# Kernel tuning notes

Measured on AMD Instinct MI355X. Metric: run time of the kernel, lower is better.

## Reference

```python
import jax, jax.numpy as jnp
import numpy as np

N = 16384      # total nodes (hits)
K = 8          # n_neighbors
NB = 8         # number of graphs in batch
IN_C = 6       # in_channels
HID = 128      # hidden_channels
NCLS = 3       # num_classes
SLOPE = 0.2    # GATv2 leaky_relu negative_slope
BIG = 1e30     # mask value for cross-graph pairs


def setup_inputs() -> dict:
    key = jax.random.key(0)
    ks = jax.random.split(key, 32)
    coord = jax.random.normal(ks[0], (N, 3), dtype=jnp.float32)
    feat = jax.random.normal(ks[1], (N, IN_C), dtype=jnp.float32)
    batch = jnp.sort(jax.random.randint(ks[2], (N,), 0, NB)).astype(jnp.int32)

    def lin_w(k, fan_in, fan_out):
        return (jax.random.normal(k, (fan_in, fan_out), dtype=jnp.float32)
                * np.float32(1.0 / np.sqrt(fan_in)))

    inp = {"coord": coord, "feat": feat, "batch": batch}
    dims = [IN_C, HID, HID]  # input dim of each of the 3 GATv2 layers
    kidx = 3
    for l, din in enumerate(dims):
        inp[f"Wl{l}"] = lin_w(ks[kidx], din, HID); kidx += 1
        inp[f"bl{l}"] = jnp.zeros((HID,), jnp.float32)
        inp[f"Wr{l}"] = lin_w(ks[kidx], din, HID); kidx += 1
        inp[f"br{l}"] = jnp.zeros((HID,), jnp.float32)
        inp[f"att{l}"] = (jax.random.normal(ks[kidx], (HID,), dtype=jnp.float32)
                          * np.float32(1.0 / np.sqrt(HID))); kidx += 1
        inp[f"bias{l}"] = jnp.zeros((HID,), jnp.float32)
    inp["Wf"] = lin_w(ks[kidx], HID, NCLS)
    inp["bf"] = jnp.zeros((NCLS,), jnp.float32)
    return inp


def knn_idx(coord, batch):
    # pairwise squared distances, masked so neighbors stay within the same graph
    d2 = jnp.sum((coord[:, None, :] - coord[None, :, :]) ** 2, axis=-1)  # [N,N]
    d2 = jnp.where(batch[:, None] == batch[None, :], d2, BIG)
    _, idx = jax.lax.top_k(-d2, K)  # [N,K] nearest (includes self at dist 0)
    return idx


def gatv2_layer(x, idx, Wl, bl, Wr, br, att, bias):
    xl = x @ Wl + bl                         # [N,H] source transform
    xr = x @ Wr + br                         # [N,H] target transform
    g = xl[idx]                              # [N,K,H] gather neighbor features
    e = jax.nn.leaky_relu(g + xr[:, None, :], SLOPE)
    logits = e @ att                         # [N,K] attention scores
    alpha = jax.nn.softmax(logits, axis=1)   # softmax over each node's K nbrs
    return jnp.einsum('nk,nkh->nh', alpha, g) + bias


def reference(coord, feat, batch,
              Wl0, bl0, Wr0, br0, att0, bias0,
              Wl1, bl1, Wr1, br1, att1, bias1,
              Wl2, bl2, Wr2, br2, att2, bias2,
              Wf, bf):
    idx = knn_idx(coord, batch)
    x = jax.nn.relu(gatv2_layer(feat, idx, Wl0, bl0, Wr0, br0, att0, bias0))
    x = jax.nn.relu(gatv2_layer(x, idx, Wl1, bl1, Wr1, br1, att1, bias1))
    x = jax.nn.relu(gatv2_layer(x, idx, Wl2, bl2, Wr2, br2, att2, bias2))
    return x @ Wf + bf
```

## Files before the change

kernel.cpp:

```cpp
#include <hip/hip_runtime.h>
#include <hip/hip_bf16.h>
#include <float.h>
#include <limits.h>

#define NNODES 16384
#define KNB 8
#define HIDC 128
#define KNN_CAP 2528

__device__ __forceinline__ float wave_sum(float x) {
  x += __int_as_float(__builtin_amdgcn_update_dpp(0, __float_as_int(x), 0xB1, 0xF, 0xF, true));
  x += __int_as_float(__builtin_amdgcn_update_dpp(0, __float_as_int(x), 0x4E, 0xF, 0xF, true));
  x += __int_as_float(__builtin_amdgcn_update_dpp(0, __float_as_int(x), 0x124, 0xF, 0xF, true));
  x += __int_as_float(__builtin_amdgcn_update_dpp(0, __float_as_int(x), 0x128, 0xF, 0xF, true));
  float r0 = __int_as_float(__builtin_amdgcn_readlane(__float_as_int(x), 0));
  float r1 = __int_as_float(__builtin_amdgcn_readlane(__float_as_int(x), 16));
  float r2 = __int_as_float(__builtin_amdgcn_readlane(__float_as_int(x), 32));
  float r3 = __int_as_float(__builtin_amdgcn_readlane(__float_as_int(x), 48));
  return (r0 + r1) + (r2 + r3);
}

__device__ __forceinline__ float wave_min_f32(float x) {
  x = fminf(x, __int_as_float(__builtin_amdgcn_update_dpp(0, __float_as_int(x), 0xB1, 0xF, 0xF, true)));
  x = fminf(x, __int_as_float(__builtin_amdgcn_update_dpp(0, __float_as_int(x), 0x4E, 0xF, 0xF, true)));
  x = fminf(x, __int_as_float(__builtin_amdgcn_update_dpp(0, __float_as_int(x), 0x124, 0xF, 0xF, true)));
  x = fminf(x, __int_as_float(__builtin_amdgcn_update_dpp(0, __float_as_int(x), 0x128, 0xF, 0xF, true)));
  float r0 = __int_as_float(__builtin_amdgcn_readlane(__float_as_int(x), 0));
  float r1 = __int_as_float(__builtin_amdgcn_readlane(__float_as_int(x), 16));
  float r2 = __int_as_float(__builtin_amdgcn_readlane(__float_as_int(x), 32));
  float r3 = __int_as_float(__builtin_amdgcn_readlane(__float_as_int(x), 48));
  return fminf(fminf(r0, r1), fminf(r2, r3));
}

__device__ __forceinline__ float dist2(float ax, float ay, float az,
                                       float bx, float by, float bz) {
  float dx = ax - bx, dy = ay - by, dz = az - bz;
  return fmaf(dz, dz, fmaf(dy, dy, dx * dx));
}

#define INS8V(_d, a0, a1, a2, a3, a4, a5, a6, a7)  \
  do {                                             \
    a7 = __builtin_amdgcn_fmed3f(_d, a6, a7);      \
    a6 = __builtin_amdgcn_fmed3f(_d, a5, a6);      \
    a5 = __builtin_amdgcn_fmed3f(_d, a4, a5);      \
    a4 = __builtin_amdgcn_fmed3f(_d, a3, a4);      \
    a3 = __builtin_amdgcn_fmed3f(_d, a2, a3);      \
    a2 = __builtin_amdgcn_fmed3f(_d, a1, a2);      \
    a1 = __builtin_amdgcn_fmed3f(_d, a0, a1);      \
    a0 = fminf(a0, _d);                            \
  } while (0)

__device__ __forceinline__ float merge_T(float l0, float l1, float l2, float l3,
                                         float l4, float l5, float l6, float l7,
                                         int lane) {
  float T = 0.f;
  #pragma unroll
  for (int r = 0; r < KNB; ++r) {
    float m = wave_min_f32(l0);
    T = m;
    unsigned long long msk = __ballot(l0 == m);
    int p = (int)__builtin_ctzll(msk);
    if (lane == p) { l0 = l1; l1 = l2; l2 = l3; l3 = l4; l4 = l5; l5 = l6; l6 = l7; l7 = FLT_MAX; }
  }
  return T;
}

__device__ void knn_global_single(const float* __restrict__ coord,
                                  float qx, float qy, float qz,
                                  int s, int e, int lane,
                                  int* __restrict__ knn_row) {
  float l0 = FLT_MAX, l1 = FLT_MAX, l2 = FLT_MAX, l3 = FLT_MAX,
        l4 = FLT_MAX, l5 = FLT_MAX, l6 = FLT_MAX, l7 = FLT_MAX;
  for (int base = s; base < e; base += 64) {
    int j = base + lane;
    bool ok = j < e;
    int jc = ok ? j : s;
    float d = dist2(coord[jc*3+0], coord[jc*3+1], coord[jc*3+2], qx, qy, qz);
    d = ok ? d : FLT_MAX;
    INS8V(d, l0, l1, l2, l3, l4, l5, l6, l7);
  }
  float T = merge_T(l0, l1, l2, l3, l4, l5, l6, l7, lane);
  unsigned long long lt = (1ull << lane) - 1ull;
  int cnt = 0;
  for (int base = s; base < e; base += 64) {
    int j = base + lane;
    bool ok = j < e;
    int jc = ok ? j : s;
    float d = dist2(coord[jc*3+0], coord[jc*3+1], coord[jc*3+2], qx, qy, qz);
    bool win = ok && (d <= T);
    unsigned long long msk = __ballot(win);
    if (msk) {
      int slot = cnt + __popcll(msk & lt);
      if (win && slot < KNB) knn_row[slot] = j;
      cnt += __popcll(msk);
    }
  }
}

__global__ void seg_kernel(const int* __restrict__ batch, int* __restrict__ seg) {
  int b = threadIdx.x;
  if (b > 8) return;
  int lo = 0, hi = NNODES;
  while (lo < hi) { int m = (lo + hi) >> 1; if (batch[m] < b) lo = m + 1; else hi = m; }
  seg[b] = lo;
}

__global__ __launch_bounds__(512, 8) void knnlin_kernel(
    const float* __restrict__ coord, const int* __restrict__ batch,
    const float* __restrict__ feat,
    const float* __restrict__ Wl0, const float* __restrict__ bl0,
    const float* __restrict__ Wr0, const float* __restrict__ br0,
    const int* __restrict__ seg,
    int* __restrict__ knn, float* __restrict__ xl, float* __restrict__ xr) {
  __shared__ float xs[KNN_CAP];
  __shared__ float ys[KNN_CAP];
  __shared__ float zs[KNN_CAP];
  int t = threadIdx.x;
  int lane = t & 63;
  int wid = t >> 6;
  int n0 = blockIdx.x * 16;

  int b0 = batch[n0];
  int blast = batch[n0 + 15];
  int smin = seg[b0];
  int emax = seg[blast + 1];
  int win_end = min(emax, smin + KNN_CAP);
  int cnt_fill = win_end - smin;

  for (int i = t; i < cnt_fill; i += 512) {
    const float* cp = coord + (size_t)(smin + i) * 3;
    xs[i] = cp[0]; ys[i] = cp[1]; zs[i] = cp[2];
  }
  __syncthreads();

  int nA = n0 + wid * 2, nB = nA + 1;
  int bA = batch[nA], bB = batch[nB];
  int sA = seg[bA], eA = seg[bA + 1];
  bool fast = (bA == bB) && (eA - smin <= KNN_CAP);

  float ax = coord[nA*3+0], ay = coord[nA*3+1], az = coord[nA*3+2];
  float bx = coord[nB*3+0], by = coord[nB*3+1], bz = coord[nB*3+2];

  if (fast) {
    int lo_i = sA - smin;
    int M = eA - sA;
    int F4 = M >> 8;

    float a0 = FLT_MAX, a1 = FLT_MAX, a2 = FLT_MAX, a3 = FLT_MAX,
          a4 = FLT_MAX, a5 = FLT_MAX, a6 = FLT_MAX, a7 = FLT_MAX;
    float b0r = FLT_MAX, b1 = FLT_MAX, b2 = FLT_MAX, b3 = FLT_MAX,
          b4 = FLT_MAX, b5 = FLT_MAX, b6 = FLT_MAX, b7 = FLT_MAX;
    {
      for (int it = 0; it < F4; ++it) {
        int base = lo_i + (it << 8) + lane;
        #pragma unroll
        for (int q = 0; q < 4; ++q) {
          int i = base + (q << 6);
          float cxv = xs[i], cyv = ys[i], czv = zs[i];
          float dA = dist2(cxv, cyv, czv, ax, ay, az);
          float dB = dist2(cxv, cyv, czv, bx, by, bz);
          INS8V(dA, a0, a1, a2, a3, a4, a5, a6, a7);
          INS8V(dB, b0r, b1, b2, b3, b4, b5, b6, b7);
        }
      }
      for (int base = F4 << 8; base < M; base += 64) {
        int lix = base + lane;
        bool ok = lix < M;
        int i = ok ? (lo_i + lix) : lo_i;
        float cxv = xs[i], cyv = ys[i], czv = zs[i];
        float dA = dist2(cxv, cyv, czv, ax, ay, az);
        float dB = dist2(cxv, cyv, czv, bx, by, bz);
        dA = ok ? dA : FLT_MAX;
        dB = ok ? dB : FLT_MAX;
        INS8V(dA, a0, a1, a2, a3, a4, a5, a6, a7);
        INS8V(dB, b0r, b1, b2, b3, b4, b5, b6, b7);
      }
    }

    float TA = merge_T(a0, a1, a2, a3, a4, a5, a6, a7, lane);
    float TB = merge_T(b0r, b1, b2, b3, b4, b5, b6, b7, lane);

    unsigned long long lt = (1ull << lane) - 1ull;
    int cntA = 0, cntB = 0;
    {
      for (int it = 0; it < F4 && (cntA < KNB || cntB < KNB); ++it) {
        int base = lo_i + (it << 8) + lane;
        int g0 = sA + (it << 8) + lane;
        #pragma unroll
        for (int q = 0; q < 4; ++q) {
          int i = base + (q << 6);
          int gidx = g0 + (q << 6);
          float cxv = xs[i], cyv = ys[i], czv = zs[i];
          float dA = dist2(cxv, cyv, czv, ax, ay, az);
          float dB = dist2(cxv, cyv, czv, bx, by, bz);
          unsigned long long mA = __ballot(dA <= TA);
          if (mA) {
            int slot = cntA + __popcll(mA & lt);
            if ((dA <= TA) && slot < KNB) knn[nA*KNB + slot] = gidx;
            cntA += __popcll(mA);
          }
          unsigned long long mB = __ballot(dB <= TB);
          if (mB) {
            int slot = cntB + __popcll(mB & lt);
            if ((dB <= TB) && slot < KNB) knn[nB*KNB + slot] = gidx;
            cntB += __popcll(mB);
          }
        }
      }
      for (int base = F4 << 8; base < M && (cntA < KNB || cntB < KNB); base += 64) {
        int lix = base + lane;
        bool ok = lix < M;
        int i = ok ? (lo_i + lix) : lo_i;
        float cxv = xs[i], cyv = ys[i], czv = zs[i];
        float dA = dist2(cxv, cyv, czv, ax, ay, az);
        float dB = dist2(cxv, cyv, czv, bx, by, bz);
        int gidx = sA + lix;
        bool wA = ok && (dA <= TA);
        bool wB = ok && (dB <= TB);
        unsigned long long mA = __ballot(wA);
        if (mA) {
          int slot = cntA + __popcll(mA & lt);
          if (wA && slot < KNB) knn[nA*KNB + slot] = gidx;
          cntA += __popcll(mA);
        }
        unsigned long long mB = __ballot(wB);
        if (mB) {
          int slot = cntB + __popcll(mB & lt);
          if (wB && slot < KNB) knn[nB*KNB + slot] = gidx;
          cntB += __popcll(mB);
        }
      }
    }
  } else {
    int sB2 = seg[bB], eB2 = seg[bB + 1];
    knn_global_single(coord, ax, ay, az, sA, eA, lane, knn + (size_t)nA * KNB);
    knn_global_single(coord, bx, by, bz, sB2, eB2, lane, knn + (size_t)nB * KNB);
  }

  {
    int cg = t & 63;
    bool isR = cg >= 32;
    const float* W  = isR ? Wr0 : Wl0;
    const float* bi = isR ? br0 : bl0;
    float* dst      = isR ? xr : xl;
    int wc = (cg & 31) * 4;
    float4 w0 = *(const float4*)(W + 0 * HIDC + wc);
    float4 w1 = *(const float4*)(W + 1 * HIDC + wc);
    float4 w2 = *(const float4*)(W + 2 * HIDC + wc);
    float4 w3 = *(const float4*)(W + 3 * HIDC + wc);
    float4 w4 = *(const float4*)(W + 4 * HIDC + wc);
    float4 w5 = *(const float4*)(W + 5 * HIDC + wc);
    float4 bb = *(const float4*)(bi + wc);
    #pragma unroll
    for (int s2 = 0; s2 < 2; ++s2) {
      int node = n0 + wid * 2 + s2;
      const float* fr = feat + (size_t)node * 6;
      float f0 = fr[0], f1 = fr[1], f2 = fr[2], f3 = fr[3], f4 = fr[4], f5 = fr[5];
      float4 acc = make_float4(0.f, 0.f, 0.f, 0.f);
      acc.x = fmaf(f0, w0.x, acc.x); acc.y = fmaf(f0, w0.y, acc.y);
      acc.z = fmaf(f0, w0.z, acc.z); acc.w = fmaf(f0, w0.w, acc.w);
      acc.x = fmaf(f1, w1.x, acc.x); acc.y = fmaf(f1, w1.y, acc.y);
      acc.z = fmaf(f1, w1.z, acc.z); acc.w = fmaf(f1, w1.w, acc.w);
      acc.x = fmaf(f2, w2.x, acc.x); acc.y = fmaf(f2, w2.y, acc.y);
      acc.z = fmaf(f2, w2.z, acc.z); acc.w = fmaf(f2, w2.w, acc.w);
      acc.x = fmaf(f3, w3.x, acc.x); acc.y = fmaf(f3, w3.y, acc.y);
      acc.z = fmaf(f3, w3.z, acc.z); acc.w = fmaf(f3, w3.w, acc.w);
      acc.x = fmaf(f4, w4.x, acc.x); acc.y = fmaf(f4, w4.y, acc.y);
      acc.z = fmaf(f4, w4.z, acc.z); acc.w = fmaf(f4, w4.w, acc.w);
      acc.x = fmaf(f5, w5.x, acc.x); acc.y = fmaf(f5, w5.y, acc.y);
      acc.z = fmaf(f5, w5.z, acc.z); acc.w = fmaf(f5, w5.w, acc.w);
      float4 o;
      o.x = acc.x + bb.x; o.y = acc.y + bb.y;
      o.z = acc.z + bb.z; o.w = acc.w + bb.w;
      *(float4*)(dst + (size_t)node * HIDC + wc) = o;
    }
  }
}

__global__ __launch_bounds__(256) void lin2_kernel(
    const float* __restrict__ x,
    const float* __restrict__ Wl, const float* __restrict__ bl,
    const float* __restrict__ Wr, const float* __restrict__ br,
    float* __restrict__ xl, float* __restrict__ xr) {
  __shared__ float xshm[16 * HIDC];
  int t = threadIdx.x;
  int node0 = blockIdx.x * 16;
  for (int i = t; i < 16 * HIDC; i += 256) xshm[i] = x[node0 * HIDC + i];
  __syncthreads();
  int cg = t & 63;
  int ng = t >> 6;
  int c0 = cg * 4;
  bool isR = (c0 >= HIDC);
  const float* W    = isR ? Wr : Wl;
  const float* bias = isR ? br : bl;
  float* dst        = isR ? xr : xl;
  int wc = isR ? (c0 - HIDC) : c0;

  float4 acc[4];
  #pragma unroll
  for (int nn = 0; nn < 4; ++nn) acc[nn] = make_float4(0.f, 0.f, 0.f, 0.f);

  for (int k0 = 0; k0 < HIDC; k0 += 4) {
    float4 xv[4];
    #pragma unroll
    for (int nn = 0; nn < 4; ++nn)
      xv[nn] = *(const float4*)&xshm[(ng * 4 + nn) * HIDC + k0];
    #pragma unroll
    for (int q = 0; q < 4; ++q) {
      float4 w = *(const float4*)(W + (size_t)(k0 + q) * HIDC + wc);
      #pragma unroll
      for (int nn = 0; nn < 4; ++nn) {
        float xq = (q == 0) ? xv[nn].x : (q == 1) ? xv[nn].y : (q == 2) ? xv[nn].z : xv[nn].w;
        acc[nn].x = fmaf(xq, w.x, acc[nn].x);
        acc[nn].y = fmaf(xq, w.y, acc[nn].y);
        acc[nn].z = fmaf(xq, w.z, acc[nn].z);
        acc[nn].w = fmaf(xq, w.w, acc[nn].w);
      }
    }
  }
  float4 b4 = *(const float4*)(bias + wc);
  #pragma unroll
  for (int nn = 0; nn < 4; ++nn) {
    int node = node0 + ng * 4 + nn;
    float4 o;
    o.x = acc[nn].x + b4.x; o.y = acc[nn].y + b4.y;
    o.z = acc[nn].z + b4.z; o.w = acc[nn].w + b4.w;
    *(float4*)(dst + (size_t)node * HIDC + wc) = o;
  }
}

template<bool FINAL>
__global__ __launch_bounds__(256) void gat_attn_kernel(
    const float* __restrict__ xl, const float* __restrict__ xr,
    const int* __restrict__ knn, const float* __restrict__ att,
    const float* __restrict__ bias, float* __restrict__ xout,
    const float* __restrict__ Wf, const float* __restrict__ bf,
    float* __restrict__ out) {
  int wid = threadIdx.x >> 6;
  int lane = threadIdx.x & 63;
  int n = blockIdx.x * 4 + wid;
  int c0 = 2 * lane, c1 = 2 * lane + 1;
  float2 xr2 = *(const float2*)(xr + (size_t)n * HIDC + c0);
  float2 a2  = *(const float2*)(att + c0);
  int myj = (lane < KNB) ? knn[n * KNB + lane] : 0;
  float g0[8], g1[8], lg[8];
  #pragma unroll
  for (int k = 0; k < 8; ++k) {
    int j = __builtin_amdgcn_readlane(myj, k);
    float2 g = *(const float2*)(xl + (size_t)j * HIDC + c0);
    g0[k] = g.x; g1[k] = g.y;
    float e0 = g.x + xr2.x; e0 = (e0 > 0.f) ? e0 : 0.2f * e0;
    float e1 = g.y + xr2.y; e1 = (e1 > 0.f) ? e1 : 0.2f * e1;
    lg[k] = wave_sum(e0 * a2.x + e1 * a2.y);
  }
  float mx = lg[0];
  #pragma unroll
  for (int k = 1; k < 8; ++k) mx = fmaxf(mx, lg[k]);
  float ssum = 0.f, w[8];
  #pragma unroll
  for (int k = 0; k < 8; ++k) { w[k] = __expf(lg[k] - mx); ssum += w[k]; }
  float inv = 1.f / ssum;
  float o0 = 0.f, o1 = 0.f;
  #pragma unroll
  for (int k = 0; k < 8; ++k) { o0 += w[k] * g0[k]; o1 += w[k] * g1[k]; }
  o0 = fmaxf(fmaf(o0, inv, bias[c0]), 0.f);
  o1 = fmaxf(fmaf(o1, inv, bias[c1]), 0.f);
  if (!FINAL) {
    float2 o; o.x = o0; o.y = o1;
    *(float2*)(xout + (size_t)n * HIDC + c0) = o;
  } else {
    #pragma unroll
    for (int cls = 0; cls < 3; ++cls) {
      float p = wave_sum(o0 * Wf[c0 * 3 + cls] + o1 * Wf[c1 * 3 + cls]);
      if (lane == 0) out[n * 3 + cls] = p + bf[cls];
    }
  }
}

extern "C" void kernel_launch(void* const* d_in, const int* in_sizes, int n_in,
                              void* d_out, int out_size, void* d_ws, size_t ws_size,
                              hipStream_t stream) {
  const float* coord = (const float*)d_in[0];
  const float* feat  = (const float*)d_in[1];
  const int*   batch = (const int*)d_in[2];
  const float* Wl0 = (const float*)d_in[3];
  const float* bl0 = (const float*)d_in[4];
  const float* Wr0 = (const float*)d_in[5];
  const float* br0 = (const float*)d_in[6];
  const float* att0  = (const float*)d_in[7];
  const float* bias0 = (const float*)d_in[8];
  const float* Wl1 = (const float*)d_in[9];
  const float* bl1 = (const float*)d_in[10];
  const float* Wr1 = (const float*)d_in[11];
  const float* br1 = (const float*)d_in[12];
  const float* att1  = (const float*)d_in[13];
  const float* bias1 = (const float*)d_in[14];
  const float* Wl2 = (const float*)d_in[15];
  const float* bl2 = (const float*)d_in[16];
  const float* Wr2 = (const float*)d_in[17];
  const float* br2 = (const float*)d_in[18];
  const float* att2  = (const float*)d_in[19];
  const float* bias2 = (const float*)d_in[20];
  const float* Wf = (const float*)d_in[21];
  const float* bf = (const float*)d_in[22];
  float* out = (float*)d_out;

  char* ws = (char*)d_ws;
  int*   knn = (int*)ws;
  float* xl  = (float*)(ws + (512 << 10));
  float* xr  = xl + (size_t)NNODES * HIDC;
  float* xb0 = xr + (size_t)NNODES * HIDC;
  float* xb1 = xb0 + (size_t)NNODES * HIDC;
  int*   seg = (int*)xb1;

  seg_kernel<<<1, 16, 0, stream>>>(batch, seg);
  knnlin_kernel<<<NNODES / 16, 512, 0, stream>>>(coord, batch, feat,
                                                 Wl0, bl0, Wr0, br0, seg, knn, xl, xr);
  gat_attn_kernel<false><<<NNODES / 4, 256, 0, stream>>>(xl, xr, knn, att0, bias0, xb0,
                                                         nullptr, nullptr, nullptr);

  lin2_kernel<<<NNODES / 16, 256, 0, stream>>>(xb0, Wl1, bl1, Wr1, br1, xl, xr);
  gat_attn_kernel<false><<<NNODES / 4, 256, 0, stream>>>(xl, xr, knn, att1, bias1, xb1,
                                                         nullptr, nullptr, nullptr);

  lin2_kernel<<<NNODES / 16, 256, 0, stream>>>(xb1, Wl2, bl2, Wr2, br2, xl, xr);
  gat_attn_kernel<true><<<NNODES / 4, 256, 0, stream>>>(xl, xr, knn, att2, bias2, nullptr,
                                                        Wf, bf, out);
}
```

Baseline: 138.2 us.

## Process four query nodes per wave in KNN to reuse LDS candidate loads

Each wave now handles four query nodes instead of two, so every candidate coordinate read from LDS is reused across four distance computations. Blocks cover 32 nodes, which halves the grid and the number of per-block LDS fills. The 4x-unrolled first-pass loop is replaced with a simple 64-stride loop, and the second pass exits early once all four queries have their K neighbours. Keeping four sorted top-8 lists per lane raises register pressure, so launch bounds drop to 4 blocks per CU, and the halved grid gives less parallelism.

Result: slower. 157.8 us (+14.1%).

```diff
diff --git a/kernel.cpp b/kernel.cpp
--- a/kernel.cpp
+++ b/kernel.cpp
@@ -105,7 +105,7 @@
   seg[b] = lo;
 }
 
-__global__ __launch_bounds__(512, 8) void knnlin_kernel(
+__global__ __launch_bounds__(512, 4) void knnlin_kernel(
     const float* __restrict__ coord, const int* __restrict__ batch,
     const float* __restrict__ feat,
     const float* __restrict__ Wl0, const float* __restrict__ bl0,
@@ -118,10 +118,10 @@
   int t = threadIdx.x;
   int lane = t & 63;
   int wid = t >> 6;
-  int n0 = blockIdx.x * 16;
+  int n0 = blockIdx.x * 32;
 
   int b0 = batch[n0];
-  int blast = batch[n0 + 15];
+  int blast = batch[n0 + 31];
   int smin = seg[b0];
   int emax = seg[blast + 1];
   int win_end = min(emax, smin + KNN_CAP);
@@ -133,108 +133,95 @@
   }
   __syncthreads();
 
-  int nA = n0 + wid * 2, nB = nA + 1;
-  int bA = batch[nA], bB = batch[nB];
-  int sA = seg[bA], eA = seg[bA + 1];
-  bool fast = (bA == bB) && (eA - smin <= KNN_CAP);
-
-  float ax = coord[nA*3+0], ay = coord[nA*3+1], az = coord[nA*3+2];
-  float bx = coord[nB*3+0], by = coord[nB*3+1], bz = coord[nB*3+2];
+  int nQ0 = n0 + wid * 4, nQ1 = nQ0 + 1, nQ2 = nQ0 + 2, nQ3 = nQ0 + 3;
+  int bQ0 = batch[nQ0], bQ3 = batch[nQ3];
+  int sA = seg[bQ0], eA = seg[bQ0 + 1];
+  bool fast = (bQ0 == bQ3) && (eA - smin <= KNN_CAP);
+
+  float q0x = coord[nQ0*3+0], q0y = coord[nQ0*3+1], q0z = coord[nQ0*3+2];
+  float q1x = coord[nQ1*3+0], q1y = coord[nQ1*3+1], q1z = coord[nQ1*3+2];
+  float q2x = coord[nQ2*3+0], q2y = coord[nQ2*3+1], q2z = coord[nQ2*3+2];
+  float q3x = coord[nQ3*3+0], q3y = coord[nQ3*3+1], q3z = coord[nQ3*3+2];
 
   if (fast) {
     int lo_i = sA - smin;
     int M = eA - sA;
-    int F4 = M >> 8;
+    int Mf = M & ~63;
 
     float a0 = FLT_MAX, a1 = FLT_MAX, a2 = FLT_MAX, a3 = FLT_MAX,
           a4 = FLT_MAX, a5 = FLT_MAX, a6 = FLT_MAX, a7 = FLT_MAX;
     float b0r = FLT_MAX, b1 = FLT_MAX, b2 = FLT_MAX, b3 = FLT_MAX,
           b4 = FLT_MAX, b5 = FLT_MAX, b6 = FLT_MAX, b7 = FLT_MAX;
-    {
-      for (int it = 0; it < F4; ++it) {
-        int base = lo_i + (it << 8) + lane;
-        #pragma unroll
-        for (int q = 0; q < 4; ++q) {
-          int i = base + (q << 6);
-          float cxv = xs[i], cyv = ys[i], czv = zs[i];
-          float dA = dist2(cxv, cyv, czv, ax, ay, az);
-          float dB = dist2(cxv, cyv, czv, bx, by, bz);
-          INS8V(dA, a0, a1, a2, a3, a4, a5, a6, a7);
-          INS8V(dB, b0r, b1, b2, b3, b4, b5, b6, b7);
-        }
-      }
-      for (int base = F4 << 8; base < M; base += 64) {
-        int lix = base + lane;
-        bool ok = lix < M;
-        int i = ok ? (lo_i + lix) : lo_i;
-        float cxv = xs[i], cyv = ys[i], czv = zs[i];
-        float dA = dist2(cxv, cyv, czv, ax, ay, az);
-        float dB = dist2(cxv, cyv, czv, bx, by, bz);
-        dA = ok ? dA : FLT_MAX;
-        dB = ok ? dB : FLT_MAX;
-        INS8V(dA, a0, a1, a2, a3, a4, a5, a6, a7);
-        INS8V(dB, b0r, b1, b2, b3, b4, b5, b6, b7);
-      }
-    }
-
-    float TA = merge_T(a0, a1, a2, a3, a4, a5, a6, a7, lane);
-    float TB = merge_T(b0r, b1, b2, b3, b4, b5, b6, b7, lane);
+    float c0r = FLT_MAX, c1 = FLT_MAX, c2 = FLT_MAX, c3 = FLT_MAX,
+          c4 = FLT_MAX, c5 = FLT_MAX, c6 = FLT_MAX, c7 = FLT_MAX;
+    float e0r = FLT_MAX, e1 = FLT_MAX, e2 = FLT_MAX, e3 = FLT_MAX,
+          e4 = FLT_MAX, e5 = FLT_MAX, e6 = FLT_MAX, e7 = FLT_MAX;
+    for (int base = 0; base < Mf; base += 64) {
+      int i = lo_i + base + lane;
+      float cxv = xs[i], cyv = ys[i], czv = zs[i];
+      float d0 = dist2(cxv, cyv, czv, q0x, q0y, q0z);
+      float d1 = dist2(cxv, cyv, czv, q1x, q1y, q1z);
+      float d2v = dist2(cxv, cyv, czv, q2x, q2y, q2z);
+      float d3 = dist2(cxv, cyv, czv, q3x, q3y, q3z);
+      INS8V(d0, a0, a1, a2, a3, a4, a5, a6, a7);
+      INS8V(d1, b0r, b1, b2, b3, b4, b5, b6, b7);
+      INS8V(d2v, c0r, c1, c2, c3, c4, c5, c6, c7);
+      INS8V(d3, e0r, e1, e2, e3, e4, e5, e6, e7);
+    }
+    if (Mf < M) {
+      int lix = Mf + lane;
+      bool ok = lix < M;
+      int i = ok ? (lo_i + lix) : lo_i;
+      float cxv = xs[i], cyv = ys[i], czv = zs[i];
+      float d0 = ok ? dist2(cxv, cyv, czv, q0x, q0y, q0z) : FLT_MAX;
+      float d1 = ok ? dist2(cxv, cyv, czv, q1x, q1y, q1z) : FLT_MAX;
+      float d2v = ok ? dist2(cxv, cyv, czv, q2x, q2y, q2z) : FLT_MAX;
+      float d3 = ok ? dist2(cxv, cyv, czv, q3x, q3y, q3z) : FLT_MAX;
+      INS8V(d0, a0, a1, a2, a3, a4, a5, a6, a7);
+      INS8V(d1, b0r, b1, b2, b3, b4, b5, b6, b7);
+      INS8V(d2v, c0r, c1, c2, c3, c4, c5, c6, c7);
+      INS8V(d3, e0r, e1, e2, e3, e4, e5, e6, e7);
+    }
+
+    float T0 = merge_T(a0, a1, a2, a3, a4, a5, a6, a7, lane);
+    float T1 = merge_T(b0r, b1, b2, b3, b4, b5, b6, b7, lane);
+    float T2 = merge_T(c0r, c1, c2, c3, c4, c5, c6, c7, lane);
+    float T3 = merge_T(e0r, e1, e2, e3, e4, e5, e6, e7, lane);
 
     unsigned long long lt = (1ull << lane) - 1ull;
-    int cntA = 0, cntB = 0;
-    {
-      for (int it = 0; it < F4 && (cntA < KNB || cntB < KNB); ++it) {
-        int base = lo_i + (it << 8) + lane;
-        int g0 = sA + (it << 8) + lane;
-        #pragma unroll
-        for (int q = 0; q < 4; ++q) {
-          int i = base + (q << 6);
-          int gidx = g0 + (q << 6);
-          float cxv = xs[i], cyv = ys[i], czv = zs[i];
-          float dA = dist2(cxv, cyv, czv, ax, ay, az);
-          float dB = dist2(cxv, cyv, czv, bx, by, bz);
-          unsigned long long mA = __ballot(dA <= TA);
-          if (mA) {
-            int slot = cntA + __popcll(mA & lt);
-            if ((dA <= TA) && slot < KNB) knn[nA*KNB + slot] = gidx;
-            cntA += __popcll(mA);
-          }
-          unsigned long long mB = __ballot(dB <= TB);
-          if (mB) {
-            int slot = cntB + __popcll(mB & lt);
-            if ((dB <= TB) && slot < KNB) knn[nB*KNB + slot] = gidx;
-            cntB += __popcll(mB);
-          }
-        }
-      }
-      for (int base = F4 << 8; base < M && (cntA < KNB || cntB < KNB); base += 64) {
-        int lix = base + lane;
-        bool ok = lix < M;
-        int i = ok ? (lo_i + lix) : lo_i;
-        float cxv = xs[i], cyv = ys[i], czv = zs[i];
-        float dA = dist2(cxv, cyv, czv, ax, ay, az);
-        float dB = dist2(cxv, cyv, czv, bx, by, bz);
-        int gidx = sA + lix;
-        bool wA = ok && (dA <= TA);
-        bool wB = ok && (dB <= TB);
-        unsigned long long mA = __ballot(wA);
-        if (mA) {
-          int slot = cntA + __popcll(mA & lt);
-          if (wA && slot < KNB) knn[nA*KNB + slot] = gidx;
-          cntA += __popcll(mA);
-        }
-        unsigned long long mB = __ballot(wB);
-        if (mB) {
-          int slot = cntB + __popcll(mB & lt);
-          if (wB && slot < KNB) knn[nB*KNB + slot] = gidx;
-          cntB += __popcll(mB);
-        }
-      }
-    }
+    int cnt0 = 0, cnt1 = 0, cnt2 = 0, cnt3 = 0;
+#define PASS2Q(dq, Tq, cntq, nq)                                   \
+    {                                                              \
+      bool w = okc && ((dq) <= (Tq));                              \
+      unsigned long long m = __ballot(w);                          \
+      if (m) {                                                     \
+        int slot = cntq + __popcll(m & lt);                        \
+        if (w && slot < KNB) knn[(size_t)(nq)*KNB + slot] = gidx;  \
+        cntq += __popcll(m);                                       \
+      }                                                            \
+    }
+    for (int base = 0; base < M; base += 64) {
+      int lix = base + lane;
+      bool okc = lix < M;
+      int i = okc ? (lo_i + lix) : lo_i;
+      int gidx = sA + lix;
+      float cxv = xs[i], cyv = ys[i], czv = zs[i];
+      float d0 = dist2(cxv, cyv, czv, q0x, q0y, q0z);
+      float d1 = dist2(cxv, cyv, czv, q1x, q1y, q1z);
+      float d2v = dist2(cxv, cyv, czv, q2x, q2y, q2z);
+      float d3 = dist2(cxv, cyv, czv, q3x, q3y, q3z);
+      PASS2Q(d0, T0, cnt0, nQ0);
+      PASS2Q(d1, T1, cnt1, nQ1);
+      PASS2Q(d2v, T2, cnt2, nQ2);
+      PASS2Q(d3, T3, cnt3, nQ3);
+      if (cnt0 >= KNB && cnt1 >= KNB && cnt2 >= KNB && cnt3 >= KNB) break;
+    }
+#undef PASS2Q
   } else {
-    int sB2 = seg[bB], eB2 = seg[bB + 1];
-    knn_global_single(coord, ax, ay, az, sA, eA, lane, knn + (size_t)nA * KNB);
-    knn_global_single(coord, bx, by, bz, sB2, eB2, lane, knn + (size_t)nB * KNB);
+    knn_global_single(coord, q0x, q0y, q0z, seg[batch[nQ0]], seg[batch[nQ0]+1], lane, knn + (size_t)nQ0 * KNB);
+    knn_global_single(coord, q1x, q1y, q1z, seg[batch[nQ1]], seg[batch[nQ1]+1], lane, knn + (size_t)nQ1 * KNB);
+    knn_global_single(coord, q2x, q2y, q2z, seg[batch[nQ2]], seg[batch[nQ2]+1], lane, knn + (size_t)nQ2 * KNB);
+    knn_global_single(coord, q3x, q3y, q3z, seg[batch[nQ3]], seg[batch[nQ3]+1], lane, knn + (size_t)nQ3 * KNB);
   }
 
   {
@@ -252,8 +239,8 @@
     float4 w5 = *(const float4*)(W + 5 * HIDC + wc);
     float4 bb = *(const float4*)(bi + wc);
     #pragma unroll
-    for (int s2 = 0; s2 < 2; ++s2) {
-      int node = n0 + wid * 2 + s2;
+    for (int s2 = 0; s2 < 4; ++s2) {
+      int node = n0 + wid * 4 + s2;
       const float* fr = feat + (size_t)node * 6;
       float f0 = fr[0], f1 = fr[1], f2 = fr[2], f3 = fr[3], f4 = fr[4], f5 = fr[5];
       float4 acc = make_float4(0.f, 0.f, 0.f, 0.f);
@@ -414,7 +401,7 @@
   int*   seg = (int*)xb1;
 
   seg_kernel<<<1, 16, 0, stream>>>(batch, seg);
-  knnlin_kernel<<<NNODES / 16, 512, 0, stream>>>(coord, batch, feat,
+  knnlin_kernel<<<NNODES / 32, 512, 0, stream>>>(coord, batch, feat,
                                                  Wl0, bl0, Wr0, br0, seg, knn, xl, xr);
   gat_attn_kernel<false><<<NNODES / 4, 256, 0, stream>>>(xl, xr, knn, att0, bias0, xb0,
                                                          nullptr, nullptr, nullptr);
```

## Fuse GAT attention with next layer's linear transforms, ping-pong buffers

Applied to the files above, without the earlier changes.

Merges each intermediate GATv2 attention step with the following layer's Wl/Wr projection into one kernel. The aggregated node features stay in shared memory instead of being written to global memory and read back, which also removes two kernel launches. Each block now handles 8 nodes instead of 16 for the linear part, so every weight row is loaded for fewer nodes. Double-buffered xl/xr arrays avoid read-after-write hazards between layers.

New measurement: 142.0 us. 2.8% more time.

```diff
diff --git a/kernel.cpp b/kernel.cpp
--- a/kernel.cpp
+++ b/kernel.cpp
@@ -277,39 +277,77 @@
   }
 }
 
-__global__ __launch_bounds__(256) void lin2_kernel(
-    const float* __restrict__ x,
+__global__ __launch_bounds__(256) void gatlin_kernel(
+    const float* __restrict__ xl_in, const float* __restrict__ xr_in,
+    const int* __restrict__ knn, const float* __restrict__ att,
+    const float* __restrict__ bias,
     const float* __restrict__ Wl, const float* __restrict__ bl,
     const float* __restrict__ Wr, const float* __restrict__ br,
-    float* __restrict__ xl, float* __restrict__ xr) {
-  __shared__ float xshm[16 * HIDC];
+    float* __restrict__ xl_out, float* __restrict__ xr_out) {
+  __shared__ float xshm[8 * HIDC];
   int t = threadIdx.x;
-  int node0 = blockIdx.x * 16;
-  for (int i = t; i < 16 * HIDC; i += 256) xshm[i] = x[node0 * HIDC + i];
+  int wid = t >> 6;
+  int lane = t & 63;
+  int n0 = blockIdx.x * 8;
+  int c0 = 2 * lane, c1 = c0 + 1;
+  float2 a2 = *(const float2*)(att + c0);
+  float2 b2 = *(const float2*)(bias + c0);
+
+  #pragma unroll
+  for (int s = 0; s < 2; ++s) {
+    int nl = wid * 2 + s;
+    int n = n0 + nl;
+    float2 xr2 = *(const float2*)(xr_in + (size_t)n * HIDC + c0);
+    int myj = (lane < KNB) ? knn[n * KNB + lane] : 0;
+    float g0[8], g1[8], lg[8];
+    #pragma unroll
+    for (int k = 0; k < 8; ++k) {
+      int j = __builtin_amdgcn_readlane(myj, k);
+      float2 g = *(const float2*)(xl_in + (size_t)j * HIDC + c0);
+      g0[k] = g.x; g1[k] = g.y;
+      float e0 = g.x + xr2.x; e0 = (e0 > 0.f) ? e0 : 0.2f * e0;
+      float e1 = g.y + xr2.y; e1 = (e1 > 0.f) ? e1 : 0.2f * e1;
+      lg[k] = wave_sum(e0 * a2.x + e1 * a2.y);
+    }
+    float mx = lg[0];
+    #pragma unroll
+    for (int k = 1; k < 8; ++k) mx = fmaxf(mx, lg[k]);
+    float ssum = 0.f, w[8];
+    #pragma unroll
+    for (int k = 0; k < 8; ++k) { w[k] = __expf(lg[k] - mx); ssum += w[k]; }
+    float inv = 1.f / ssum;
+    float o0 = 0.f, o1 = 0.f;
+    #pragma unroll
+    for (int k = 0; k < 8; ++k) { o0 += w[k] * g0[k]; o1 += w[k] * g1[k]; }
+    o0 = fmaxf(fmaf(o0, inv, b2.x), 0.f);
+    o1 = fmaxf(fmaf(o1, inv, b2.y), 0.f);
+    float2 o; o.x = o0; o.y = o1;
+    *(float2*)(&xshm[nl * HIDC + c0]) = o;
+  }
   __syncthreads();
+
   int cg = t & 63;
   int ng = t >> 6;
-  int c0 = cg * 4;
-  bool isR = (c0 >= HIDC);
+  bool isR = cg >= 32;
   const float* W    = isR ? Wr : Wl;
-  const float* bias = isR ? br : bl;
-  float* dst        = isR ? xr : xl;
-  int wc = isR ? (c0 - HIDC) : c0;
-
-  float4 acc[4];
-  #pragma unroll
-  for (int nn = 0; nn < 4; ++nn) acc[nn] = make_float4(0.f, 0.f, 0.f, 0.f);
+  const float* bi   = isR ? br : bl;
+  float* dst        = isR ? xr_out : xl_out;
+  int wc = (cg & 31) * 4;
+
+  float4 acc[2];
+  acc[0] = make_float4(0.f, 0.f, 0.f, 0.f);
+  acc[1] = make_float4(0.f, 0.f, 0.f, 0.f);
 
   for (int k0 = 0; k0 < HIDC; k0 += 4) {
-    float4 xv[4];
-    #pragma unroll
-    for (int nn = 0; nn < 4; ++nn)
-      xv[nn] = *(const float4*)&xshm[(ng * 4 + nn) * HIDC + k0];
+    float4 xv[2];
+    #pragma unroll
+    for (int nn = 0; nn < 2; ++nn)
+      xv[nn] = *(const float4*)&xshm[(ng * 2 + nn) * HIDC + k0];
     #pragma unroll
     for (int q = 0; q < 4; ++q) {
       float4 w = *(const float4*)(W + (size_t)(k0 + q) * HIDC + wc);
       #pragma unroll
-      for (int nn = 0; nn < 4; ++nn) {
+      for (int nn = 0; nn < 2; ++nn) {
         float xq = (q == 0) ? xv[nn].x : (q == 1) ? xv[nn].y : (q == 2) ? xv[nn].z : xv[nn].w;
         acc[nn].x = fmaf(xq, w.x, acc[nn].x);
         acc[nn].y = fmaf(xq, w.y, acc[nn].y);
@@ -318,10 +356,10 @@
       }
     }
   }
-  float4 b4 = *(const float4*)(bias + wc);
-  #pragma unroll
-  for (int nn = 0; nn < 4; ++nn) {
-    int node = node0 + ng * 4 + nn;
+  float4 b4 = *(const float4*)(bi + wc);
+  #pragma unroll
+  for (int nn = 0; nn < 2; ++nn) {
+    int node = n0 + ng * 2 + nn;
     float4 o;
     o.x = acc[nn].x + b4.x; o.y = acc[nn].y + b4.y;
     o.z = acc[nn].z + b4.z; o.w = acc[nn].w + b4.w;
@@ -329,11 +367,10 @@
   }
 }
 
-template<bool FINAL>
-__global__ __launch_bounds__(256) void gat_attn_kernel(
+__global__ __launch_bounds__(256) void gat_final_kernel(
     const float* __restrict__ xl, const float* __restrict__ xr,
     const int* __restrict__ knn, const float* __restrict__ att,
-    const float* __restrict__ bias, float* __restrict__ xout,
+    const float* __restrict__ bias,
     const float* __restrict__ Wf, const float* __restrict__ bf,
     float* __restrict__ out) {
   int wid = threadIdx.x >> 6;
@@ -365,15 +402,10 @@
   for (int k = 0; k < 8; ++k) { o0 += w[k] * g0[k]; o1 += w[k] * g1[k]; }
   o0 = fmaxf(fmaf(o0, inv, bias[c0]), 0.f);
   o1 = fmaxf(fmaf(o1, inv, bias[c1]), 0.f);
-  if (!FINAL) {
-    float2 o; o.x = o0; o.y = o1;
-    *(float2*)(xout + (size_t)n * HIDC + c0) = o;
-  } else {
-    #pragma unroll
-    for (int cls = 0; cls < 3; ++cls) {
-      float p = wave_sum(o0 * Wf[c0 * 3 + cls] + o1 * Wf[c1 * 3 + cls]);
-      if (lane == 0) out[n * 3 + cls] = p + bf[cls];
-    }
+  #pragma unroll
+  for (int cls = 0; cls < 3; ++cls) {
+    float p = wave_sum(o0 * Wf[c0 * 3 + cls] + o1 * Wf[c1 * 3 + cls]);
+    if (lane == 0) out[n * 3 + cls] = p + bf[cls];
   }
 }
 
@@ -407,23 +439,19 @@
 
   char* ws = (char*)d_ws;
   int*   knn = (int*)ws;
-  float* xl  = (float*)(ws + (512 << 10));
-  float* xr  = xl + (size_t)NNODES * HIDC;
-  float* xb0 = xr + (size_t)NNODES * HIDC;
-  float* xb1 = xb0 + (size_t)NNODES * HIDC;
-  int*   seg = (int*)xb1;
+  float* xlA = (float*)(ws + (512 << 10));
+  float* xrA = xlA + (size_t)NNODES * HIDC;
+  float* xlB = xrA + (size_t)NNODES * HIDC;
+  float* xrB = xlB + (size_t)NNODES * HIDC;
+  int*   seg = (int*)(xrB + (size_t)NNODES * HIDC);
 
   seg_kernel<<<1, 16, 0, stream>>>(batch, seg);
   knnlin_kernel<<<NNODES / 16, 512, 0, stream>>>(coord, batch, feat,
-                                                 Wl0, bl0, Wr0, br0, seg, knn, xl, xr);
-  gat_attn_kernel<false><<<NNODES / 4, 256, 0, stream>>>(xl, xr, knn, att0, bias0, xb0,
-                                                         nullptr, nullptr, nullptr);
-
-  lin2_kernel<<<NNODES / 16, 256, 0, stream>>>(xb0, Wl1, bl1, Wr1, br1, xl, xr);
-  gat_attn_kernel<false><<<NNODES / 4, 256, 0, stream>>>(xl, xr, knn, att1, bias1, xb1,
-                                                         nullptr, nullptr, nullptr);
-
-  lin2_kernel<<<NNODES / 16, 256, 0, stream>>>(xb1, Wl2, bl2, Wr2, br2, xl, xr);
-  gat_attn_kernel<true><<<NNODES / 4, 256, 0, stream>>>(xl, xr, knn, att2, bias2, nullptr,
-                                                        Wf, bf, out);
-}
+                                                 Wl0, bl0, Wr0, br0, seg, knn, xlA, xrA);
+  gatlin_kernel<<<NNODES / 8, 256, 0, stream>>>(xlA, xrA, knn, att0, bias0,
+                                                Wl1, bl1, Wr1, br1, xlB, xrB);
+  gatlin_kernel<<<NNODES / 8, 256, 0, stream>>>(xlB, xrB, knn, att1, bias1,
+                                                Wl2, bl2, Wr2, br2, xlA, xrA);
+  gat_final_kernel<<<NNODES / 4, 256, 0, stream>>>(xlA, xrA, knn, att2, bias2,
+                                                   Wf, bf, out);
+}
```
